# Kernel tuning notes

Measured on AMD Instinct MI355X. Metric: run time of the kernel, lower is better.

The kernel has to match this reference:

```python
import jax, jax.numpy as jnp
import numpy as np

B, C, T, H, W, TS = 4, 512, 2048, 8, 16, 1000
D = C // H  # head_dim = 64
SCALE = D ** -0.5


def _conv1x1(w, b, z):
    # torch Conv1d(dim, dim, 1): (B,C,T) -> (B,C,T)
    return jnp.einsum('oc,bct->bot', w, z) + b[None, :, None]


def _linear(w, b, z):
    # torch Linear: z @ w.T + b, w is (out,in)
    return z @ w.T + b


def _rope(x, cos, sin):
    # x: (B,H,T,D); cos/sin: (T, D//2) broadcast over (B,H)
    x1, x2 = x[..., ::2], x[..., 1::2]
    r = jnp.stack([x1 * cos - x2 * sin, x1 * sin + x2 * cos], axis=-1)
    return r.reshape(x.shape)


def _local(x, cond, qw, qb, kw, kb, vw, vb, ow, ob):
    q = _conv1x1(qw, qb, x)
    k = _conv1x1(kw, kb, cond)
    v = _conv1x1(vw, vb, cond)
    pl = W // 2
    pr = W - pl - 1
    kp = jnp.pad(k, ((0, 0), (0, 0), (pl, pr)))
    vp = jnp.pad(v, ((0, 0), (0, 0), (pl, pr)))
    idx = jnp.arange(T)[:, None] + jnp.arange(W)[None, :]  # (T,W)
    ku = kp[:, :, idx].reshape(B, H, D, T, W)
    vu = vp[:, :, idx].reshape(B, H, D, T, W)
    qh = q.reshape(B, H, D, T)
    dots = jnp.einsum('bhdt,bhdtw->bhtw', qh, ku) * SCALE
    attn = jax.nn.softmax(dots, axis=-1)
    out = jnp.einsum('bhtw,bhdtw->bhdt', attn, vu)
    # faithful to torch: permute(0,1,3,2).contiguous().view(B,C,T)
    out = out.transpose(0, 1, 3, 2).reshape(B, C, T)
    return _conv1x1(ow, ob, out)


def _global(xg, cg, qw, qb, kw, kb, vw, vb, ow, ob):
    # xg, cg: (B,T,C)
    q = _linear(qw, qb, xg).reshape(B, T, H, D).transpose(0, 2, 1, 3)
    k = _linear(kw, kb, cg).reshape(B, T, H, D).transpose(0, 2, 1, 3)
    v = _linear(vw, vb, cg).reshape(B, T, H, D).transpose(0, 2, 1, 3)
    inv_freq = 1.0 / (10000.0 ** (jnp.arange(0, D, 2, dtype=jnp.float32) / D))
    pos = jnp.arange(T, dtype=jnp.float32)
    sinus = pos[:, None] * inv_freq[None, :]  # (T, D//2)
    cos, sin = jnp.cos(sinus), jnp.sin(sinus)
    q = _rope(q, cos, sin)
    k = _rope(k, cos, sin)
    dots = jnp.einsum('bhqd,bhkd->bhqk', q, k) * SCALE
    attn = jax.nn.softmax(dots, axis=-1)
    out = jnp.einsum('bhqk,bhkd->bhqd', attn, v)
    out = out.transpose(0, 2, 1, 3).reshape(B, T, C)
    return _linear(ow, ob, out)


def setup_inputs() -> dict:
    key = jax.random.key(0)
    ks = jax.random.split(key, 20)
    pm = lambda k: jax.random.normal(k, (C, C), dtype=jnp.float32) * 0.02
    pb = lambda k: jax.random.normal(k, (C,), dtype=jnp.float32) * 0.02
    return {
        'x': jax.random.normal(ks[0], (B, C, T), dtype=jnp.float32),
        'cond': jax.random.normal(ks[1], (B, C, T), dtype=jnp.float32),
        't': jax.random.randint(ks[2], (B,), 0, TS),
        'lq_w': pm(ks[3]), 'lq_b': pb(ks[4]),
        'lk_w': pm(ks[5]), 'lk_b': pb(ks[6]),
        'lv_w': pm(ks[7]), 'lv_b': pb(ks[8]),
        'lo_w': pm(ks[9]), 'lo_b': pb(ks[10]),
        'gq_w': pm(ks[11]), 'gq_b': pb(ks[12]),
        'gk_w': pm(ks[13]), 'gk_b': pb(ks[14]),
        'gv_w': pm(ks[15]), 'gv_b': pb(ks[16]),
        'go_w': pm(ks[17]), 'go_b': pb(ks[18]),
    }


def reference(x, cond, t, lq_w, lq_b, lk_w, lk_b, lv_w, lv_b, lo_w, lo_b,
              gq_w, gq_b, gk_w, gk_b, gv_w, gv_b, go_w, go_b):
    ctx_local = _local(x, cond, lq_w, lq_b, lk_w, lk_b, lv_w, lv_b, lo_w, lo_b)
    ctx_global = _global(x.transpose(0, 2, 1), cond.transpose(0, 2, 1),
                         gq_w, gq_b, gk_w, gk_b, gv_w, gv_b, go_w, go_b)
    ctx_global = ctx_global.transpose(0, 2, 1)  # (B,C,T)
    t_norm = t.astype(jnp.float32) / jnp.float32(TS - 1)
    a_g = (1.0 - t_norm)[:, None, None]
    a_l = t_norm[:, None, None]
    return jnp.sqrt(a_g) * ctx_global + jnp.sqrt(a_l) * ctx_local
```

## Files before the change

### kernel.cpp

```cpp
#include <hip/hip_runtime.h>
#include <math.h>

#define BB 4
#define CC 512
#define TT 2048
#define HH 8
#define DD 64

static constexpr float SCALE = 0.125f;
static constexpr float QK_SCALE_LOG2 = 0.125f * 1.4426950408889634f;

typedef __attribute__((ext_vector_type(8)))  short  short8;
typedef __attribute__((ext_vector_type(4)))  float  f32x4;
typedef __attribute__((ext_vector_type(16))) float  f32x16;
typedef __attribute__((ext_vector_type(2)))  unsigned int u32x2;

static __device__ __forceinline__ ushort f2bf(float f) {
    uint u = __float_as_uint(f);
    uint r = (u + 0x7fffu + ((u >> 16) & 1u)) >> 16;
    return (ushort)r;
}
static __device__ __forceinline__ float bf2f(ushort u) {
    return __uint_as_float((uint)u << 16);
}

typedef unsigned int u32;
typedef u32 __attribute__((address_space(1))) gu32;
typedef u32 __attribute__((address_space(3))) lu32;
static __device__ __forceinline__ void gload_lds16(const void* g, void* l) {
    __builtin_amdgcn_global_load_lds((const gu32*)g, (lu32*)l, 16, 0, 0);
}

__global__ __launch_bounds__(256)
void prep_kernel(const float* __restrict__ x, const float* __restrict__ cond,
                 const float* w0, const float* w1, const float* w2, const float* w3,
                 const float* w4, const float* w5, const float* w6, const float* w7,
                 ushort* __restrict__ wbf, ushort* __restrict__ wc,
                 ushort* __restrict__ xtb, ushort* __restrict__ ctb,
                 float* __restrict__ ctab, float* __restrict__ stab)
{
    __shared__ ushort L[64][66];
    int bid = blockIdx.x;
    const int tid = threadIdx.x;

    if (bid < 256) {
        int idx = bid * 256 + tid;
        int i = idx >> 11;
        int t = idx & 2047;
        float ex   = (2.0f * (float)i) / 64.0f;
        float invf = powf(10000.0f, -ex);
        float ang  = (float)t * invf;
        ctab[idx] = cosf(ang);
        stab[idx] = sinf(ang);
        return;
    }
    bid -= 256;
    if (bid < 2048) {
        const float* srcs[8] = {w0, w1, w2, w3, w4, w5, w6, w7};
        int wi = bid >> 8;
        int idx = ((bid & 255) * 256 + tid) * 4;
        float4 v = *(const float4*)&srcs[wi][idx];
        uint lo = (uint)f2bf(v.x) | ((uint)f2bf(v.y) << 16);
        uint hi = (uint)f2bf(v.z) | ((uint)f2bf(v.w) << 16);
        uint2 pk = make_uint2(lo, hi);
        if (wi < 6) {
            *(uint2*)&wbf[(size_t)wi * 262144 + idx] = pk;
        } else {
            int row = idx >> 9, col = idx & 511;
            *(uint2*)&wc[(size_t)row * 1024 + (wi - 6) * 512 + col] = pk;
        }
        return;
    }
    bid -= 2048;
    const int z = bid >> 8;
    const int r = bid & 255;
    const float* in = (z < 4) ? x : cond;
    ushort* outp    = (z < 4) ? xtb : ctb;
    const int b = z & 3;
    const int t0 = (r & 31) * 64, c0 = (r >> 5) * 64;
    const float* inb = in + (size_t)b * CC * TT;
    ushort* outb = outp + (size_t)b * TT * CC;
    const int lc = tid >> 6;
    const int lt = tid & 63;
    #pragma unroll
    for (int i = 0; i < 16; i++) {
        int c = i * 4 + lc;
        L[c][lt] = f2bf(inb[(size_t)(c0 + c) * TT + t0 + lt]);
    }
    __syncthreads();
    #pragma unroll
    for (int i = 0; i < 16; i++) {
        int t = i * 4 + lc;
        outb[(size_t)(t0 + t) * CC + c0 + lt] = L[lt][t];
    }
}

__global__ __launch_bounds__(256)
void transpose_bf16_kernel(const ushort* __restrict__ in, ushort* __restrict__ AG)
{
    __shared__ ushort L[64][66];
    const int t0 = blockIdx.x * 64, c0 = blockIdx.y * 64, b = blockIdx.z;
    const ushort* inb = in + (size_t)b * CC * TT;
    ushort* outb = AG + (size_t)b * TT * 1024;
    const int lc = threadIdx.x >> 6;
    const int lt = threadIdx.x & 63;
    #pragma unroll
    for (int i = 0; i < 16; i++) {
        int c = i * 4 + lc;
        L[c][lt] = inb[(size_t)(c0 + c) * TT + t0 + lt];
    }
    __syncthreads();
    #pragma unroll
    for (int i = 0; i < 16; i++) {
        int t = i * 4 + lc;
        outb[(size_t)(t0 + t) * 1024 + c0 + lt] = L[lt][t];
    }
}

#define GEMM_BODY(Wp, XTp, KD, NB)                                                  \
    __shared__ __align__(16) ushort As[2][128][32];                                 \
    __shared__ __align__(16) ushort Bs[2][NB][32];                                  \
    const int tid  = threadIdx.x;                                                   \
    const int wid  = tid >> 6;                                                      \
    const int lane = tid & 63;                                                      \
    const int x  = lane & 15;                                                       \
    const int gq = lane >> 4;                                                       \
    const int wm = wid >> 1, wn = wid & 1;                                          \
    const int m0 = blockIdx.y * 128;                                                \
    const int n0 = blockIdx.x * NB;                                                 \
    const int srow = lane >> 2;                                                     \
    const int sblk = lane & 3;                                                      \
    f32x4 acc[4][NB / 32];                                                          \
    _Pragma("unroll")                                                               \
    for (int i = 0; i < 4; i++)                                                     \
        _Pragma("unroll")                                                           \
        for (int j = 0; j < NB / 32; j++) acc[i][j] = (f32x4){0.f, 0.f, 0.f, 0.f};  \
    auto stage = [&](int bf, int k0) {                                              \
        _Pragma("unroll")                                                           \
        for (int c = 0; c < 2; c++) {                                               \
            int row = c * 64 + wid * 16 + srow;                                     \
            int dbk = sblk ^ ((row >> 1) & 3);                                      \
            gload_lds16(&Wp[(size_t)(m0 + row) * KD + k0 + dbk * 8],                \
                        &As[bf][c * 64 + wid * 16][0]);                             \
            if (c * 64 < NB)                                                        \
                gload_lds16(&XTp[(size_t)(n0 + row) * KD + k0 + dbk * 8],           \
                            &Bs[bf][c * 64 + wid * 16][0]);                         \
        }                                                                           \
    };                                                                              \
    stage(0, 0);                                                                    \
    __syncthreads();                                                                \
    for (int ks = 0; ks < (KD) / 32; ks++) {                                        \
        int cur = ks & 1;                                                           \
        if (ks < (KD) / 32 - 1) stage(cur ^ 1, (ks + 1) * 32);                      \
        short8 aF[4], bF[NB / 32];                                                  \
        _Pragma("unroll")                                                           \
        for (int mi = 0; mi < 4; mi++) {                                            \
            int row = wm * 64 + mi * 16 + x;                                        \
            aF[mi] = *(const short8*)&As[cur][row][(gq ^ ((row >> 1) & 3)) * 8];    \
        }                                                                           \
        _Pragma("unroll")                                                           \
        for (int nj = 0; nj < NB / 32; nj++) {                                      \
            int row = wn * (NB / 2) + nj * 16 + x;                                  \
            bF[nj] = *(const short8*)&Bs[cur][row][(gq ^ ((row >> 1) & 3)) * 8];    \
        }                                                                           \
        _Pragma("unroll")                                                           \
        for (int mi = 0; mi < 4; mi++)                                              \
            _Pragma("unroll")                                                       \
            for (int nj = 0; nj < NB / 32; nj++)                                    \
                acc[mi][nj] = __builtin_amdgcn_mfma_f32_16x16x32_bf16(aF[mi], bF[nj], acc[mi][nj], 0, 0, 0); \
        __syncthreads();                                                            \
    }

__global__ __launch_bounds__(256)
void gemm6_kernel(const ushort* __restrict__ wbase,
                  const float* __restrict__ b0, const float* __restrict__ b1, const float* __restrict__ b2,
                  const float* __restrict__ b3, const float* __restrict__ b4, const float* __restrict__ b5,
                  const ushort* __restrict__ xtb, const ushort* __restrict__ ctb,
                  ushort* __restrict__ y0, ushort* __restrict__ y1, ushort* __restrict__ y2,
                  ushort* __restrict__ y3, ushort* __restrict__ y4, ushort* __restrict__ y5,
                  const float* __restrict__ ctab, const float* __restrict__ stab)
{
    __shared__ __align__(16) ushort SMEM[16384];
    ushort (*As)[128][32] = (ushort(*)[128][32])&SMEM[0];
    ushort (*Bs)[128][32] = (ushort(*)[128][32])&SMEM[8192];

    const int z = blockIdx.z;
    const ushort* Wp  = wbase + (size_t)z * 262144;
    const float* bias = (z == 0) ? b0 : (z == 1) ? b1 : (z == 2) ? b2 : (z == 3) ? b3 : (z == 4) ? b4 : b5;
    const ushort* XTp = (z == 0 || z == 3) ? xtb : ctb;
    ushort* Y = (z == 0) ? y0 : (z == 1) ? y1 : (z == 2) ? y2 : (z == 3) ? y3 : (z == 4) ? y4 : y5;
    const bool do_rope = (z == 3 || z == 4);
    const bool swp = (z == 5);
    const float qscale = (z == 3) ? QK_SCALE_LOG2 : 1.0f;

    const int tid  = threadIdx.x;
    const int wid  = tid >> 6;
    const int lane = tid & 63;
    const int x  = lane & 15;
    const int gq = lane >> 4;
    const int wm = wid >> 1, wn = wid & 1;
    const int m0 = blockIdx.y * 128;
    const int n0 = blockIdx.x * 128;
    const int srow = lane >> 2;
    const int sblk = lane & 3;

    f32x4 acc[4][4];
    #pragma unroll
    for (int i = 0; i < 4; i++)
        #pragma unroll
        for (int j = 0; j < 4; j++) acc[i][j] = (f32x4){0.f, 0.f, 0.f, 0.f};

    auto stage = [&](int bf, int k0) {
        #pragma unroll
        for (int c = 0; c < 2; c++) {
            int row = c * 64 + wid * 16 + srow;
            int dbk = sblk ^ ((row >> 1) & 3);
            gload_lds16(&Wp[(size_t)(m0 + row) * 512 + k0 + dbk * 8],
                        &As[bf][c * 64 + wid * 16][0]);
            gload_lds16(&XTp[(size_t)(n0 + row) * 512 + k0 + dbk * 8],
                        &Bs[bf][c * 64 + wid * 16][0]);
        }
    };
    stage(0, 0);
    __syncthreads();

    for (int ks = 0; ks < 16; ks++) {
        int cur = ks & 1;
        if (ks < 15) stage(cur ^ 1, (ks + 1) * 32);
        short8 aF[4], bF[4];
        #pragma unroll
        for (int mi = 0; mi < 4; mi++) {
            int row = wm * 64 + mi * 16 + x;
            aF[mi] = *(const short8*)&As[cur][row][(gq ^ ((row >> 1) & 3)) * 8];
        }
        #pragma unroll
        for (int nj = 0; nj < 4; nj++) {
            int row = wn * 64 + nj * 16 + x;
            bF[nj] = *(const short8*)&Bs[cur][row][(gq ^ ((row >> 1) & 3)) * 8];
        }
        if (swp) {
            #pragma unroll
            for (int mi = 0; mi < 4; mi++)
                #pragma unroll
                for (int nj = 0; nj < 4; nj++)
                    acc[mi][nj] = __builtin_amdgcn_mfma_f32_16x16x32_bf16(bF[nj], aF[mi], acc[mi][nj], 0, 0, 0);
        } else {
            #pragma unroll
            for (int mi = 0; mi < 4; mi++)
                #pragma unroll
                for (int nj = 0; nj < 4; nj++)
                    acc[mi][nj] = __builtin_amdgcn_mfma_f32_16x16x32_bf16(aF[mi], bF[nj], acc[mi][nj], 0, 0, 0);
        }
        __syncthreads();
    }

    if (!swp) {
        #pragma unroll
        for (int mi = 0; mi < 4; mi++) {
            const int cL = wm * 64 + mi * 16 + 4 * gq;
            const int mb = m0 + cL;
            float bv[4];
            #pragma unroll
            for (int r = 0; r < 4; r++) bv[r] = bias[mb + r];
            #pragma unroll
            for (int nj = 0; nj < 4; nj++) {
                const int tL = wn * 64 + nj * 16 + x;
                const int tt = (n0 + tL) & 2047;
                f32x4 v = acc[mi][nj];
                v[0] += bv[0]; v[1] += bv[1]; v[2] += bv[2]; v[3] += bv[3];
                if (do_rope) {
                    const int i0 = (mb & 63) >> 1;
                    float c0 = ctab[(size_t)i0 * 2048 + tt],       s0 = stab[(size_t)i0 * 2048 + tt];
                    float c1 = ctab[(size_t)(i0 + 1) * 2048 + tt], s1 = stab[(size_t)(i0 + 1) * 2048 + tt];
                    float e0 = (v[0] * c0 - v[1] * s0) * qscale;
                    float e1 = (v[0] * s0 + v[1] * c0) * qscale;
                    float e2 = (v[2] * c1 - v[3] * s1) * qscale;
                    float e3 = (v[2] * s1 + v[3] * c1) * qscale;
                    v[0] = e0; v[1] = e1; v[2] = e2; v[3] = e3;
                }
                uint lo = (uint)f2bf(v[0]) | ((uint)f2bf(v[1]) << 16);
                uint hi = (uint)f2bf(v[2]) | ((uint)f2bf(v[3]) << 16);
                const int blk = (cL >> 3) ^ (tL & 7);
                *(uint2*)&SMEM[tL * 128 + blk * 8 + (gq & 1) * 4] = make_uint2(lo, hi);
            }
        }
    } else {
        #pragma unroll
        for (int mi = 0; mi < 4; mi++) {
            const int cL = wm * 64 + mi * 16 + x;
            const float bv = bias[m0 + cL];
            #pragma unroll
            for (int nj = 0; nj < 4; nj++) {
                const int tL = wn * 64 + nj * 16 + 4 * gq;
                f32x4 v = acc[mi][nj];
                uint lo = (uint)f2bf(v[0] + bv) | ((uint)f2bf(v[1] + bv) << 16);
                uint hi = (uint)f2bf(v[2] + bv) | ((uint)f2bf(v[3] + bv) << 16);
                const int blk = (tL >> 3) ^ (cL & 7);
                *(uint2*)&SMEM[cL * 128 + blk * 8 + (gq & 1) * 4] = make_uint2(lo, hi);
            }
        }
    }
    __syncthreads();

    if (z <= 3) {
        #pragma unroll
        for (int s = 0; s < 8; s++) {
            const int chunk = s * 256 + tid;
            const int row = chunk >> 4;
            const int blk = chunk & 15;
            uint4 val = *(const uint4*)&SMEM[row * 128 + ((blk ^ (row & 7)) << 3)];
            *(uint4*)&Y[(size_t)(n0 + row) * 512 + m0 + blk * 8] = val;
        }
    } else if (z == 4) {
        const int bidx = n0 >> 11;
        #pragma unroll
        for (int s = 0; s < 8; s++) {
            const int chunk = s * 256 + tid;
            const int row = chunk & 127;
            const int blk = chunk >> 7;
            uint4 val = *(const uint4*)&SMEM[row * 128 + ((blk ^ (row & 7)) << 3)];
            const int tt = (n0 + row) & 2047;
            const int kt = tt >> 6, tk = tt & 63, sb = tk >> 5, qh = tk & 31;
            const int c = m0 + blk * 8;
            const int hh = (c >> 6) & 7, d = c & 63;
            const int kap = d >> 4, hb = (d >> 3) & 1;
            size_t off = (size_t)(bidx * 8 + hh) * 131072
                       + (size_t)(((((kt * 2 + sb) * 4 + kap) * 2 + hb) * 32 + qh) * 8);
            *(uint4*)&Y[off] = val;
        }
    } else {
        const int bidx = n0 >> 11;
        #pragma unroll
        for (int s = 0; s < 8; s++) {
            const int chunk = s * 256 + tid;
            const int rowc = chunk & 127;
            const int blk = chunk >> 7;
            uint4 val = *(const uint4*)&SMEM[rowc * 128 + ((blk ^ (rowc & 7)) << 3)];
            const int c = m0 + rowc;
            const int hh = (c >> 6) & 7, d = c & 63;
            const int qh = d & 31, db = (d >> 5) & 1;
            const int tt0 = (n0 + blk * 8) & 2047;
            const int kt = tt0 >> 6, kk = tt0 & 63;
            const int kc = kk >> 4, hb = (kk >> 3) & 1;
            size_t off = (size_t)(bidx * 8 + hh) * 131072
                       + (size_t)(((((kt * 2 + db) * 4 + kc) * 2 + hb) * 32 + qh) * 8);
            *(uint4*)&Y[off] = val;
        }
    }
}

__global__ __launch_bounds__(256)
void gemm_comb_kernel(const ushort* __restrict__ Wp,
                      const float* __restrict__ bl, const float* __restrict__ bg,
                      const ushort* __restrict__ XTp, float* __restrict__ Y,
                      const int* __restrict__ tarr)
{
    GEMM_BODY(Wp, XTp, 1024, 64)

    const int bidx = (n0 + wn * 32) >> 11;
    float tn = (float)tarr[bidx] / 999.0f;
    float sl = sqrtf(tn), sg = sqrtf(1.0f - tn);

    #pragma unroll
    for (int mi = 0; mi < 4; mi++) {
        const int mb = m0 + wm * 64 + mi * 16 + 4 * gq;
        float bv[4];
        #pragma unroll
        for (int r = 0; r < 4; r++) bv[r] = sl * bl[mb + r] + sg * bg[mb + r];
        #pragma unroll
        for (int nj = 0; nj < 2; nj++) {
            const int tt = (n0 + wn * 32 + nj * 16 + x) & 2047;
            f32x4 v = acc[mi][nj];
            #pragma unroll
            for (int r = 0; r < 4; r++)
                Y[((size_t)bidx * 512 + mb + r) * 2048 + tt] = v[r] + bv[r];
        }
    }
}

__global__ __launch_bounds__(256)
void local_attn_kernel(const ushort* __restrict__ qt, const ushort* __restrict__ kt,
                       const ushort* __restrict__ vt, ushort* __restrict__ outb,
                       const int* __restrict__ tarr)
{
    int gidx = blockIdx.x * 256 + threadIdx.x;
    int t  = gidx & (TT - 1);
    int bh = gidx >> 11;
    int h  = bh & (HH - 1);
    int b  = bh >> 3;
    const size_t rb = (size_t)b * TT;
    const int co = h * DD;
    const float wl = sqrtf((float)tarr[b] / 999.0f);

    float qf[64];
    {
        const ushort* qp = qt + (rb + t) * 512 + co;
        #pragma unroll
        for (int i = 0; i < 8; i++) {
            short8 v = *(const short8*)&qp[i * 8];
            #pragma unroll
            for (int j = 0; j < 8; j++) qf[i * 8 + j] = bf2f((ushort)v[j]);
        }
    }

    int koff[16]; float msk[16];
    #pragma unroll
    for (int w = 0; w < 16; w++) {
        int kidx = t + w - 8;
        msk[w]  = (kidx >= 0 && kidx < TT) ? 1.0f : 0.0f;
        koff[w] = min(max(kidx, 0), TT - 1);
    }

    float dots[16];
    #pragma unroll
    for (int w = 0; w < 16; w++) {
        const ushort* kp = kt + (rb + koff[w]) * 512 + co;
        float d0 = 0.f, d1 = 0.f;
        #pragma unroll
        for (int i = 0; i < 8; i++) {
            short8 v = *(const short8*)&kp[i * 8];
            #pragma unroll
            for (int j = 0; j < 8; j += 2) {
                d0 = fmaf(qf[i * 8 + j],     bf2f((ushort)v[j]),     d0);
                d1 = fmaf(qf[i * 8 + j + 1], bf2f((ushort)v[j + 1]), d1);
            }
        }
        dots[w] = d0 + d1;
    }

    float m = -1e30f;
    #pragma unroll
    for (int w = 0; w < 16; w++) { dots[w] = dots[w] * SCALE * msk[w]; m = fmaxf(m, dots[w]); }
    float p[16], s = 0.f;
    #pragma unroll
    for (int w = 0; w < 16; w++) { p[w] = __expf(dots[w] - m); s += p[w]; }
    float inv = wl / s;
    #pragma unroll
    for (int w = 0; w < 16; w++) p[w] *= msk[w] * inv;

    float oa[64];
    #pragma unroll
    for (int d = 0; d < 64; d++) oa[d] = 0.f;
    #pragma unroll
    for (int w = 0; w < 16; w++) {
        const ushort* vp = vt + (rb + koff[w]) * 512 + co;
        #pragma unroll
        for (int i = 0; i < 8; i++) {
            short8 v = *(const short8*)&vp[i * 8];
            #pragma unroll
            for (int j = 0; j < 8; j++)
                oa[i * 8 + j] = fmaf(p[w], bf2f((ushort)v[j]), oa[i * 8 + j]);
        }
    }

    ushort* op = outb + ((size_t)b * CC + co + (t >> 5)) * TT + (size_t)(t & 31) * DD;
    #pragma unroll
    for (int i = 0; i < 16; i++) {
        uint lo = (uint)f2bf(oa[i * 4 + 0]) | ((uint)f2bf(oa[i * 4 + 1]) << 16);
        uint hi = (uint)f2bf(oa[i * 4 + 2]) | ((uint)f2bf(oa[i * 4 + 3]) << 16);
        *(uint2*)&op[i * 4] = make_uint2(lo, hi);
    }
}

__global__ __launch_bounds__(256)
void flash_global_kernel(const ushort* __restrict__ qtd, const ushort* __restrict__ KT,
                         const ushort* __restrict__ VT, ushort* __restrict__ AG,
                         const int* __restrict__ tarr)
{
    __shared__ __align__(16) ushort Ks[2][4096];
    __shared__ __align__(16) ushort Vs[2][4096];

    const int tid  = threadIdx.x;
    const int w    = tid >> 6;
    const int lane = tid & 63;
    const int qh   = lane & 31;
    const int h    = lane >> 5;

    const int bid = blockIdx.x;
    const int sw  = (bid & 7) * 64 + (bid >> 3);
    const int qt  = sw & 15;
    const int p   = sw >> 4;
    const int hh  = p & 7, b = p >> 3;

    const size_t kvbase = (size_t)p * 131072;
    const size_t btd    = (size_t)b * TT;
    const int q_glob = qt * 128 + w * 32 + qh;
    const float sg_mix = sqrtf(1.0f - (float)tarr[b] / 999.0f);

    const ushort* Kb = KT + kvbase;
    const ushort* Vb = VT + kvbase;

    short8 aQ[4];
    {
        const ushort* qrow = qtd + (btd + q_glob) * 512 + hh * 64;
        #pragma unroll
        for (int kap = 0; kap < 4; kap++)
            aQ[kap] = *(const short8*)&qrow[kap * 16 + h * 8];
    }

    f32x16 oacc[2];
    #pragma unroll
    for (int d = 0; d < 2; d++)
        #pragma unroll
        for (int r = 0; r < 16; r++) oacc[d][r] = 0.f;
    float l_run = 0.0f;

    const ushort* kA = Kb + (size_t)(2 * w) * 512 + lane * 8;
    const ushort* vA = Vb + (size_t)(2 * w) * 512 + lane * 8;

    auto issue = [&](int buf, int kt) {
        const size_t off = (size_t)kt * 4096;
        gload_lds16(kA + off,       &Ks[buf][(2 * w) * 512]);
        gload_lds16(kA + off + 512, &Ks[buf][(2 * w + 1) * 512]);
        gload_lds16(vA + off,       &Vs[buf][(2 * w) * 512]);
        gload_lds16(vA + off + 512, &Vs[buf][(2 * w + 1) * 512]);
    };
    issue(0, 0);

    int cur = 0;
    for (int kt = 0; kt < 32; kt++) {
        __syncthreads();
        if (kt < 31) issue(cur ^ 1, kt + 1);

        const ushort* KsC = &Ks[cur][0];
        const ushort* VsC = &Vs[cur][0];

        f32x16 ST[2];
        #pragma unroll
        for (int sb = 0; sb < 2; sb++)
            #pragma unroll
            for (int r = 0; r < 16; r++) ST[sb][r] = 0.f;
        __builtin_amdgcn_s_setprio(1);
        #pragma unroll
        for (int sb = 0; sb < 2; sb++)
            #pragma unroll
            for (int kap = 0; kap < 4; kap++) {
                short8 aK = *(const short8*)&KsC[(sb * 4 + kap) * 512 + lane * 8];
                ST[sb] = __builtin_amdgcn_mfma_f32_32x32x16_bf16(aK, aQ[kap], ST[sb], 0, 0, 0);
            }
        __builtin_amdgcn_s_setprio(0);

        float s0 = 0.f, s1 = 0.f, s2 = 0.f, s3 = 0.f;
        #pragma unroll
        for (int sb = 0; sb < 2; sb++)
            #pragma unroll
            for (int r = 0; r < 16; r += 4) {
                ST[sb][r + 0] = __builtin_amdgcn_exp2f(ST[sb][r + 0]);
                ST[sb][r + 1] = __builtin_amdgcn_exp2f(ST[sb][r + 1]);
                ST[sb][r + 2] = __builtin_amdgcn_exp2f(ST[sb][r + 2]);
                ST[sb][r + 3] = __builtin_amdgcn_exp2f(ST[sb][r + 3]);
                s0 += ST[sb][r + 0]; s1 += ST[sb][r + 1];
                s2 += ST[sb][r + 2]; s3 += ST[sb][r + 3];
            }
        l_run += (s0 + s1) + (s2 + s3);

        short8 bP[4];
        #pragma unroll
        for (int sb = 0; sb < 2; sb++)
            #pragma unroll
            for (int kcp = 0; kcp < 2; kcp++) {
                const int rb2 = kcp * 8;
                uint ca, cb, cc, cd;
                asm("v_cvt_pk_bf16_f32 %0, %1, %2" : "=v"(ca) : "v"(ST[sb][rb2 + 0]), "v"(ST[sb][rb2 + 1]));
                asm("v_cvt_pk_bf16_f32 %0, %1, %2" : "=v"(cb) : "v"(ST[sb][rb2 + 2]), "v"(ST[sb][rb2 + 3]));
                asm("v_cvt_pk_bf16_f32 %0, %1, %2" : "=v"(cc) : "v"(ST[sb][rb2 + 4]), "v"(ST[sb][rb2 + 5]));
                asm("v_cvt_pk_bf16_f32 %0, %1, %2" : "=v"(cd) : "v"(ST[sb][rb2 + 6]), "v"(ST[sb][rb2 + 7]));
                u32x2 r1 = __builtin_amdgcn_permlane32_swap(ca, cc, false, false);
                u32x2 r2 = __builtin_amdgcn_permlane32_swap(cb, cd, false, false);
                uint4 bu = make_uint4(r1[0], r2[0], r1[1], r2[1]);
                bP[sb * 2 + kcp] = __builtin_bit_cast(short8, bu);
            }

        __builtin_amdgcn_s_setprio(1);
        #pragma unroll
        for (int db = 0; db < 2; db++)
            #pragma unroll
            for (int kc = 0; kc < 4; kc++) {
                short8 aV = *(const short8*)&VsC[(db * 4 + kc) * 512 + lane * 8];
                oacc[db] = __builtin_amdgcn_mfma_f32_32x32x16_bf16(aV, bP[kc], oacc[db], 0, 0, 0);
            }
        __builtin_amdgcn_s_setprio(0);
        cur ^= 1;
    }

    float ltot = l_run + __shfl_xor(l_run, 32);
    float inv = sg_mix / ltot;
    ushort* agrow = AG + (btd + q_glob) * 1024 + 512 + hh * 64;
    #pragma unroll
    for (int db = 0; db < 2; db++)
        #pragma unroll
        for (int rq = 0; rq < 4; rq++) {
            const int d0 = db * 32 + rq * 8 + h * 4;
            uint lo = (uint)f2bf(oacc[db][rq * 4 + 0] * inv) | ((uint)f2bf(oacc[db][rq * 4 + 1] * inv) << 16);
            uint hi = (uint)f2bf(oacc[db][rq * 4 + 2] * inv) | ((uint)f2bf(oacc[db][rq * 4 + 3] * inv) << 16);
            *(uint2*)&agrow[d0] = make_uint2(lo, hi);
        }
}

extern "C" void kernel_launch(void* const* d_in, const int* in_sizes, int n_in,
                              void* d_out, int out_size, void* d_ws, size_t ws_size,
                              hipStream_t stream)
{
    const float* x    = (const float*)d_in[0];
    const float* cond = (const float*)d_in[1];
    const int*   tarr = (const int*)d_in[2];
    const float* lq_w = (const float*)d_in[3];
    const float* lq_b = (const float*)d_in[4];
    const float* lk_w = (const float*)d_in[5];
    const float* lk_b = (const float*)d_in[6];
    const float* lv_w = (const float*)d_in[7];
    const float* lv_b = (const float*)d_in[8];
    const float* lo_w = (const float*)d_in[9];
    const float* lo_b = (const float*)d_in[10];
    const float* gq_w = (const float*)d_in[11];
    const float* gq_b = (const float*)d_in[12];
    const float* gk_w = (const float*)d_in[13];
    const float* gk_b = (const float*)d_in[14];
    const float* gv_w = (const float*)d_in[15];
    const float* gv_b = (const float*)d_in[16];
    const float* go_w = (const float*)d_in[17];
    const float* go_b = (const float*)d_in[18];
    float* out = (float*)d_out;

    const size_t N = (size_t)BB * CC * TT;
    char* w = (char*)d_ws;
    ushort* xtb = (ushort*)w; w += N * 2;
    ushort* ctb = (ushort*)w; w += N * 2;
    ushort* lq  = (ushort*)w; w += N * 2;
    ushort* lk  = (ushort*)w; w += N * 2;
    ushort* lv  = (ushort*)w; w += N * 2;
    ushort* gqb = (ushort*)w; w += N * 2;
    ushort* ktb = (ushort*)w; w += N * 2;
    ushort* vtb = (ushort*)w; w += N * 2;
    ushort* scr = (ushort*)w; w += N * 2;
    ushort* AG  = (ushort*)w; w += (size_t)BB * TT * 1024 * 2;
    ushort* wbf = (ushort*)w; w += (size_t)6 * 512 * 512 * 2;
    ushort* wc  = (ushort*)w; w += (size_t)512 * 1024 * 2;
    float* ctab = (float*)w;  w += (size_t)32 * 2048 * 4;
    float* stab = (float*)w;

    dim3 blk(256);

    prep_kernel<<<dim3(4352), blk, 0, stream>>>(x, cond,
                                                lq_w, lk_w, lv_w, gq_w, gk_w, gv_w, lo_w, go_w,
                                                wbf, wc, xtb, ctb, ctab, stab);

    gemm6_kernel<<<dim3(64, 4, 6), blk, 0, stream>>>(wbf, lq_b, lk_b, lv_b, gq_b, gk_b, gv_b,
                                                     xtb, ctb, lq, lk, lv, gqb, ktb, vtb, ctab, stab);

    local_attn_kernel<<<dim3(BB * HH * TT / 256), blk, 0, stream>>>(lq, lk, lv, scr, tarr);
    transpose_bf16_kernel<<<dim3(32, 8, BB), blk, 0, stream>>>(scr, AG);

    flash_global_kernel<<<dim3(512), blk, 0, stream>>>(gqb, ktb, vtb, AG, tarr);

    gemm_comb_kernel<<<dim3(128, 4), blk, 0, stream>>>(wc, lo_b, go_b, AG, out, tarr);
}
```

Measured before the change: 173.9 us.

## Split KV range across two thread groups in global flash attention block

Each block of the global attention kernel now runs 512 threads in two groups. Each group processes half of the key/value tiles with its own double-buffered LDS staging, so the serial loop is half as long. Group 1 then writes its partial output accumulators and row sums to LDS, and group 0 adds them before normalising and storing. This raises waves per CU and shortens the per-block critical path. The cost is an extra LDS reduction, more LDS per block and more register pressure at the larger block size. The partial results can be summed directly only because the softmax uses no running max.

```diff
diff --git a/kernel.cpp b/kernel.cpp
--- a/kernel.cpp
+++ b/kernel.cpp
@@ -462,16 +462,18 @@
     }
 }
 
-__global__ __launch_bounds__(256)
+__global__ __launch_bounds__(512)
 void flash_global_kernel(const ushort* __restrict__ qtd, const ushort* __restrict__ KT,
                          const ushort* __restrict__ VT, ushort* __restrict__ AG,
                          const int* __restrict__ tarr)
 {
-    __shared__ __align__(16) ushort Ks[2][4096];
-    __shared__ __align__(16) ushort Vs[2][4096];
+    __shared__ __align__(16) ushort Ks[2][2][4096];
+    __shared__ __align__(16) ushort Vs[2][2][4096];
 
     const int tid  = threadIdx.x;
-    const int w    = tid >> 6;
+    const int grp  = tid >> 8;
+    const int t8   = tid & 255;
+    const int w    = t8 >> 6;
     const int lane = tid & 63;
     const int qh   = lane & 31;
     const int h    = lane >> 5;
@@ -482,14 +484,11 @@
     const int p   = sw >> 4;
     const int hh  = p & 7, b = p >> 3;
 
-    const size_t kvbase = (size_t)p * 131072;
+    const size_t kvbase = (size_t)p * 131072 + (size_t)grp * (16 * 4096);
     const size_t btd    = (size_t)b * TT;
     const int q_glob = qt * 128 + w * 32 + qh;
     const float sg_mix = sqrtf(1.0f - (float)tarr[b] / 999.0f);
 
-    const ushort* Kb = KT + kvbase;
-    const ushort* Vb = VT + kvbase;
-
     short8 aQ[4];
     {
         const ushort* qrow = qtd + (btd + q_glob) * 512 + hh * 64;
@@ -505,25 +504,25 @@
         for (int r = 0; r < 16; r++) oacc[d][r] = 0.f;
     float l_run = 0.0f;
 
-    const ushort* kA = Kb + (size_t)(2 * w) * 512 + lane * 8;
-    const ushort* vA = Vb + (size_t)(2 * w) * 512 + lane * 8;
+    const ushort* kA = KT + kvbase + (size_t)(2 * w) * 512 + lane * 8;
+    const ushort* vA = VT + kvbase + (size_t)(2 * w) * 512 + lane * 8;
 
     auto issue = [&](int buf, int kt) {
         const size_t off = (size_t)kt * 4096;
-        gload_lds16(kA + off,       &Ks[buf][(2 * w) * 512]);
-        gload_lds16(kA + off + 512, &Ks[buf][(2 * w + 1) * 512]);
-        gload_lds16(vA + off,       &Vs[buf][(2 * w) * 512]);
-        gload_lds16(vA + off + 512, &Vs[buf][(2 * w + 1) * 512]);
+        gload_lds16(kA + off,       &Ks[grp][buf][(2 * w) * 512]);
+        gload_lds16(kA + off + 512, &Ks[grp][buf][(2 * w + 1) * 512]);
+        gload_lds16(vA + off,       &Vs[grp][buf][(2 * w) * 512]);
+        gload_lds16(vA + off + 512, &Vs[grp][buf][(2 * w + 1) * 512]);
     };
     issue(0, 0);
 
     int cur = 0;
-    for (int kt = 0; kt < 32; kt++) {
+    for (int kt = 0; kt < 16; kt++) {
         __syncthreads();
-        if (kt < 31) issue(cur ^ 1, kt + 1);
-
-        const ushort* KsC = &Ks[cur][0];
-        const ushort* VsC = &Vs[cur][0];
+        if (kt < 15) issue(cur ^ 1, kt + 1);
+
+        const ushort* KsC = &Ks[grp][cur][0];
+        const ushort* VsC = &Vs[grp][cur][0];
 
         f32x16 ST[2];
         #pragma unroll
@@ -583,18 +582,40 @@
         cur ^= 1;
     }
 
-    float ltot = l_run + __shfl_xor(l_run, 32);
-    float inv = sg_mix / ltot;
-    ushort* agrow = AG + (btd + q_glob) * 1024 + 512 + hh * 64;
-    #pragma unroll
-    for (int db = 0; db < 2; db++)
-        #pragma unroll
-        for (int rq = 0; rq < 4; rq++) {
-            const int d0 = db * 32 + rq * 8 + h * 4;
-            uint lo = (uint)f2bf(oacc[db][rq * 4 + 0] * inv) | ((uint)f2bf(oacc[db][rq * 4 + 1] * inv) << 16);
-            uint hi = (uint)f2bf(oacc[db][rq * 4 + 2] * inv) | ((uint)f2bf(oacc[db][rq * 4 + 3] * inv) << 16);
-            *(uint2*)&agrow[d0] = make_uint2(lo, hi);
-        }
+    __syncthreads();
+    f32x4* OP = (f32x4*)&Ks[0][0][0];
+    float* LP = (float*)&Vs[0][0][0];
+    if (grp == 1) {
+        #pragma unroll
+        for (int j = 0; j < 8; j++)
+            OP[j * 256 + t8] = (f32x4){oacc[j >> 2][(j & 3) * 4 + 0], oacc[j >> 2][(j & 3) * 4 + 1],
+                                       oacc[j >> 2][(j & 3) * 4 + 2], oacc[j >> 2][(j & 3) * 4 + 3]};
+        LP[t8] = l_run;
+    }
+    __syncthreads();
+    if (grp == 0) {
+        #pragma unroll
+        for (int j = 0; j < 8; j++) {
+            f32x4 o = OP[j * 256 + t8];
+            oacc[j >> 2][(j & 3) * 4 + 0] += o[0];
+            oacc[j >> 2][(j & 3) * 4 + 1] += o[1];
+            oacc[j >> 2][(j & 3) * 4 + 2] += o[2];
+            oacc[j >> 2][(j & 3) * 4 + 3] += o[3];
+        }
+        l_run += LP[t8];
+        float ltot = l_run + __shfl_xor(l_run, 32);
+        float inv = sg_mix / ltot;
+        ushort* agrow = AG + (btd + q_glob) * 1024 + 512 + hh * 64;
+        #pragma unroll
+        for (int db = 0; db < 2; db++)
+            #pragma unroll
+            for (int rq = 0; rq < 4; rq++) {
+                const int d0 = db * 32 + rq * 8 + h * 4;
+                uint lo = (uint)f2bf(oacc[db][rq * 4 + 0] * inv) | ((uint)f2bf(oacc[db][rq * 4 + 1] * inv) << 16);
+                uint hi = (uint)f2bf(oacc[db][rq * 4 + 2] * inv) | ((uint)f2bf(oacc[db][rq * 4 + 3] * inv) << 16);
+                *(uint2*)&agrow[d0] = make_uint2(lo, hi);
+            }
+    }
 }
 
 extern "C" void kernel_launch(void* const* d_in, const int* in_sizes, int n_in,
@@ -651,7 +672,7 @@
     local_attn_kernel<<<dim3(BB * HH * TT / 256), blk, 0, stream>>>(lq, lk, lv, scr, tarr);
     transpose_bf16_kernel<<<dim3(32, 8, BB), blk, 0, stream>>>(scr, AG);
 
-    flash_global_kernel<<<dim3(512), blk, 0, stream>>>(gqb, ktb, vtb, AG, tarr);
+    flash_global_kernel<<<dim3(512), dim3(512), 0, stream>>>(gqb, ktb, vtb, AG, tarr);
 
     gemm_comb_kernel<<<dim3(128, 4), blk, 0, stream>>>(wc, lo_b, go_b, AG, out, tarr);
 }
```

Result: faster. 166.7 us (-4.2%).
